# Optimization experiments

Measured on AMD Instinct MI355X. Metric: run time of the kernel, lower is better.

## Reference

```python
import jax, jax.numpy as jnp
import numpy as np

NUM_LEVELS = 4
SEARCH_RADIUS = 4
EPS = 1e-12  # torch F.normalize eps


def _avg_pool2d(x, s):
    # avg pool with kernel=stride=s over last two dims (exact, since H,W divisible by s)
    lead = x.shape[:-2]
    H, W = x.shape[-2], x.shape[-1]
    x = x.reshape(*lead, H // s, s, W // s, s)
    return x.mean(axis=(-3, -1))


def _l2_normalize(x, axis):
    n = jnp.sqrt(jnp.sum(x * x, axis=axis, keepdims=True))
    return x / jnp.maximum(n, EPS)


def _compute_correlation(query, values, radius):
    # query: [B,C,H,W], values: [B,N,C,H,W] -> [B,N,H,W,(2r+1)^2]
    q = _l2_normalize(query, axis=1)
    v = _l2_normalize(values, axis=2)
    corrs = []
    for dy in range(-radius, radius + 1):
        for dx in range(-radius, radius + 1):
            vs = v if (dy == 0 and dx == 0) else jnp.roll(v, (dy, dx), axis=(-2, -1))
            corrs.append(jnp.einsum('bchw,bnchw->bnhw', q, vs))
    return jnp.stack(corrs, axis=-1)


def setup_inputs() -> dict:
    key = jax.random.key(0)
    k1, k2, k3, k4 = jax.random.split(key, 4)
    B, N, C, H, W = 2, 4, 128, 160, 160
    Co = C // 2
    return {
        'query_feat': jax.random.normal(k1, (B, C, H, W), dtype=jnp.float32),
        'value_feats': jax.random.normal(k2, (B, N, C, H, W), dtype=jnp.float32),
        'proj_w': jax.random.normal(k3, (Co, C), dtype=jnp.float32) * (1.0 / np.sqrt(C)),
        'proj_b': jax.random.normal(k4, (Co,), dtype=jnp.float32) * 0.01,
    }


def reference(query_feat, value_feats, proj_w, proj_b):
    # 1x1 conv projection C -> C//2
    q = jnp.einsum('oc,bchw->bohw', proj_w, query_feat) + proj_b[None, :, None, None]
    v = jnp.einsum('oc,bnchw->bnohw', proj_w, value_feats) + proj_b[None, None, :, None, None]
    outs = []
    for level in range(NUM_LEVELS):
        scale = 2 ** level
        radius = max(1, SEARCH_RADIUS // scale)
        if scale > 1:
            q_l = _avg_pool2d(q, scale)
            v_l = _avg_pool2d(v, scale)
        else:
            q_l, v_l = q, v
        outs.append(_compute_correlation(q_l, v_l, radius))
    return tuple(outs)
```

## Files before the change

### kernel.cpp

```cpp
#include <hip/hip_runtime.h>


typedef _Float16 f16;
typedef _Float16 f16x4 __attribute__((ext_vector_type(4)));
typedef _Float16 f16x8 __attribute__((ext_vector_type(8)));
typedef float f32x4 __attribute__((ext_vector_type(4)));

#define EPSN 1e-12f

__global__ __launch_bounds__(256) void prep_weights(
    const float* __restrict__ wt, f16* __restrict__ wh) {
  int gid = blockIdx.x * 256 + threadIdx.x;
  float4 w = *(const float4*)(wt + gid * 4);
  f16x4 h;
  h[0] = (f16)w.x; h[1] = (f16)w.y; h[2] = (f16)w.z; h[3] = (f16)w.w;
  *(f16x4*)(wh + gid * 4) = h;
}

#define LROW 68
#define WS 136

__global__ __launch_bounds__(256, 3) void proj_pool(
    const float* __restrict__ xq, const float* __restrict__ xv,
    const f16* __restrict__ wh, const float* __restrict__ bias,
    f16* __restrict__ h0, f16* __restrict__ h1,
    f16* __restrict__ h2, f16* __restrict__ h3, int P) {
  __shared__ float xs[128 * LROW];
  __shared__ f16 wsh[64 * WS];
  float* accbuf = (float*)wsh;
  float* l3buf = xs;

  int bid = blockIdx.x;
  int img = bid / 400;
  int t = bid - img * 400;
  int ty = t / 20, tx = t - ty * 20;
  int py0 = ty * 8, px0 = tx * 8;
  const float* xsrc = (img < 2) ? (xq + (size_t)img * 128 * P)
                                : (xv + (size_t)(img - 2) * 128 * P);

  int tid = threadIdx.x;
  int lane = tid & 63;
  int wv = tid >> 6;
  int cl = lane & 15;
  int quad = lane >> 4;

  for (int m = tid; m < 1024; m += 256) {
    int o = m >> 4, kk = (m & 15) * 8;
    *(f16x8*)(wsh + o * WS + kk) = *(const f16x8*)(wh + o * 128 + kk);
  }

  {
    int cb = tid >> 4;
    int sub = tid & 15;
    int row = sub >> 1, hf = sub & 1;
#pragma unroll
    for (int i = 0; i < 8; ++i) {
      int c = cb + 16 * i;
      float4 v = *(const float4*)(xsrc + (size_t)c * P + (py0 + row) * 160 + px0 + hf * 4);
      int p = row * 8 + hf * 4;
      int x = (p + 8 * ((c >> 3) & 3)) & 63;
      *(float4*)(xs + c * LROW + x) = v;
    }
  }
  __syncthreads();

  f32x4 acc[4];
#pragma unroll
  for (int m = 0; m < 4; ++m) acc[m] = (f32x4)0.f;

  int pxl = wv * 16 + cl;
  int xr = (pxl + 8 * quad) & 63;

#pragma unroll
  for (int kc = 0; kc < 4; ++kc) {
    f16x8 bfr;
#pragma unroll
    for (int k = 0; k < 8; ++k) {
      int c = kc * 32 + quad * 8 + k;
      bfr[k] = (f16)xs[c * LROW + xr];
    }
    f16x8 afr[4];
#pragma unroll
    for (int mt = 0; mt < 4; ++mt)
      afr[mt] = *(const f16x8*)(wsh + (mt * 16 + cl) * WS + kc * 32 + quad * 8);
#pragma unroll
    for (int mt = 0; mt < 4; ++mt)
      acc[mt] = __builtin_amdgcn_mfma_f32_16x16x32_f16(afr[mt], bfr, acc[mt], 0, 0, 0);
  }

  float4 bi[4];
#pragma unroll
  for (int mt = 0; mt < 4; ++mt) bi[mt] = *(const float4*)(bias + mt * 16 + quad * 4);

  __syncthreads();

  float ss = 0.f;
#pragma unroll
  for (int mt = 0; mt < 4; ++mt) {
    acc[mt][0] += bi[mt].x;
    acc[mt][1] += bi[mt].y;
    acc[mt][2] += bi[mt].z;
    acc[mt][3] += bi[mt].w;
    *(float4*)(accbuf + pxl * LROW + mt * 16 + quad * 4) =
        make_float4(acc[mt][0], acc[mt][1], acc[mt][2], acc[mt][3]);
#pragma unroll
    for (int r = 0; r < 4; ++r) ss = fmaf(acc[mt][r], acc[mt][r], ss);
  }
  ss += __shfl_xor(ss, 16, 64);
  ss += __shfl_xor(ss, 32, 64);
  float s = 1.0f / fmaxf(sqrtf(ss), EPSN);
  {
    int gp = (py0 + (pxl >> 3)) * 160 + px0 + (pxl & 7);
    size_t base = ((size_t)img * P + gp) * 64;
#pragma unroll
    for (int mt = 0; mt < 4; ++mt) {
      f16x4 hn;
      hn[0] = (f16)(acc[mt][0] * s);
      hn[1] = (f16)(acc[mt][1] * s);
      hn[2] = (f16)(acc[mt][2] * s);
      hn[3] = (f16)(acc[mt][3] * s);
      *(f16x4*)(h0 + base + mt * 16 + quad * 4) = hn;
    }
  }
  __syncthreads();

  int r2 = wv >> 1, c2 = wv & 1;
  int g = quad, c4 = cl;
  int r1 = 2 * r2 + (g >> 1), c1 = 2 * c2 + (g & 1);
  int p00 = (2 * r1) * 8 + 2 * c1;

  float4 s00 = *(const float4*)(accbuf + p00 * LROW + c4 * 4);
  float4 s01 = *(const float4*)(accbuf + (p00 + 1) * LROW + c4 * 4);
  float4 s10 = *(const float4*)(accbuf + (p00 + 8) * LROW + c4 * 4);
  float4 s11 = *(const float4*)(accbuf + (p00 + 9) * LROW + c4 * 4);
  float4 v1;
  v1.x = 0.25f * (s00.x + s01.x + s10.x + s11.x);
  v1.y = 0.25f * (s00.y + s01.y + s10.y + s11.y);
  v1.z = 0.25f * (s00.z + s01.z + s10.z + s11.z);
  v1.w = 0.25f * (s00.w + s01.w + s10.w + s11.w);

  {
    float s1 = fmaf(v1.x, v1.x, fmaf(v1.y, v1.y, fmaf(v1.z, v1.z, v1.w * v1.w)));
    s1 += __shfl_xor(s1, 1, 64);
    s1 += __shfl_xor(s1, 2, 64);
    s1 += __shfl_xor(s1, 4, 64);
    s1 += __shfl_xor(s1, 8, 64);
    float sc = 1.0f / fmaxf(sqrtf(s1), EPSN);
    f16x4 h;
    h[0] = (f16)(v1.x * sc); h[1] = (f16)(v1.y * sc);
    h[2] = (f16)(v1.z * sc); h[3] = (f16)(v1.w * sc);
    *(f16x4*)(h1 + ((size_t)(img * 80 + ty * 4 + r1) * 80 + tx * 4 + c1) * 64 + c4 * 4) = h;
  }

  float4 q2v;
  q2v.x = v1.x + __shfl_xor(v1.x, 16, 64);
  q2v.y = v1.y + __shfl_xor(v1.y, 16, 64);
  q2v.z = v1.z + __shfl_xor(v1.z, 16, 64);
  q2v.w = v1.w + __shfl_xor(v1.w, 16, 64);
  q2v.x += __shfl_xor(q2v.x, 32, 64);
  q2v.y += __shfl_xor(q2v.y, 32, 64);
  q2v.z += __shfl_xor(q2v.z, 32, 64);
  q2v.w += __shfl_xor(q2v.w, 32, 64);
  q2v.x *= 0.25f; q2v.y *= 0.25f; q2v.z *= 0.25f; q2v.w *= 0.25f;

  {
    float s2 = fmaf(q2v.x, q2v.x, fmaf(q2v.y, q2v.y, fmaf(q2v.z, q2v.z, q2v.w * q2v.w)));
    s2 += __shfl_xor(s2, 1, 64);
    s2 += __shfl_xor(s2, 2, 64);
    s2 += __shfl_xor(s2, 4, 64);
    s2 += __shfl_xor(s2, 8, 64);
    float sc = 1.0f / fmaxf(sqrtf(s2), EPSN);
    if (g == 0) {
      f16x4 h;
      h[0] = (f16)(q2v.x * sc); h[1] = (f16)(q2v.y * sc);
      h[2] = (f16)(q2v.z * sc); h[3] = (f16)(q2v.w * sc);
      *(f16x4*)(h2 + ((size_t)(img * 40 + ty * 2 + r2) * 40 + tx * 2 + c2) * 64 + c4 * 4) = h;
      *(float4*)(l3buf + (wv * 16 + c4) * 4) = q2v;
    }
  }
  __syncthreads();

  if (tid < 16) {
    float4 a0 = *(const float4*)(l3buf + (0 * 16 + tid) * 4);
    float4 a1 = *(const float4*)(l3buf + (1 * 16 + tid) * 4);
    float4 a2 = *(const float4*)(l3buf + (2 * 16 + tid) * 4);
    float4 a3 = *(const float4*)(l3buf + (3 * 16 + tid) * 4);
    float4 q3;
    q3.x = 0.25f * (a0.x + a1.x + a2.x + a3.x);
    q3.y = 0.25f * (a0.y + a1.y + a2.y + a3.y);
    q3.z = 0.25f * (a0.z + a1.z + a2.z + a3.z);
    q3.w = 0.25f * (a0.w + a1.w + a2.w + a3.w);
    float s3 = fmaf(q3.x, q3.x, fmaf(q3.y, q3.y, fmaf(q3.z, q3.z, q3.w * q3.w)));
    s3 += __shfl_xor(s3, 1, 64);
    s3 += __shfl_xor(s3, 2, 64);
    s3 += __shfl_xor(s3, 4, 64);
    s3 += __shfl_xor(s3, 8, 64);
    float sc = 1.0f / fmaxf(sqrtf(s3), EPSN);
    f16x4 h;
    h[0] = (f16)(q3.x * sc); h[1] = (f16)(q3.y * sc);
    h[2] = (f16)(q3.z * sc); h[3] = (f16)(q3.w * sc);
    *(f16x4*)(h3 + ((size_t)(img * 20 + ty) * 20 + tx) * 64 + tid * 4) = h;
  }
}

template <int R>
__global__ __launch_bounds__(256, 4) void corr_mfma(
    const f16* __restrict__ qh, const f16* __restrict__ vh,
    float* __restrict__ out, int H, int W, int T) {
  constexpr int D = 2 * R + 1, DD = D * D;
  constexpr int PS = (DD + 3) & ~3;
  __shared__ float lw[4 * 16 * PS];

  int bn = blockIdx.x & 7;
  int wv = threadIdx.x >> 6;
  int widx = (blockIdx.x >> 3) * 4 + wv;
  int h = widx / T;
  int wt = widx - h * T;
  int lane = threadIdx.x & 63;
  int cl = lane & 15, quad = lane >> 4;
  int b = bn >> 2;
  int w0 = wt * 16;
  float* lwv = lw + wv * 16 * PS;

  int ap = w0 + cl; if (ap >= W) ap = W - 1;
  const f16* qp = qh + ((size_t)(b * H + h) * W + ap) * 64 + quad * 8;
  f16x8 a0 = *(const f16x8*)qp;
  f16x8 a1 = *(const f16x8*)(qp + 32);

  int c0 = w0 - R + cl; if (c0 < 0) c0 += W; if (c0 >= W) c0 -= W;
  int c1 = w0 + R + cl; if (c1 >= W) c1 -= W;
  int b0off = c0 * 64 + quad * 8;
  int b1off = c1 * 64 + quad * 8;

  int rbase = quad * 4;
  int base_dxi = rbase - cl + ((quad < 2) ? 2 * R : 0);

  for (int dyi = 0; dyi < D; ++dyi) {
    int h2 = h - dyi + R; if (h2 < 0) h2 += H; else if (h2 >= H) h2 -= H;
    const f16* vrow = vh + ((size_t)(bn * H + h2) * W) * 64;
    f16x8 b0a = *(const f16x8*)(vrow + b0off);
    f16x8 b0b = *(const f16x8*)(vrow + b0off + 32);
    f16x8 b1a = *(const f16x8*)(vrow + b1off);
    f16x8 b1b = *(const f16x8*)(vrow + b1off + 32);
    f32x4 A0 = __builtin_amdgcn_mfma_f32_16x16x32_f16(a0, b0a, (f32x4)0.f, 0, 0, 0);
    A0 = __builtin_amdgcn_mfma_f32_16x16x32_f16(a1, b0b, A0, 0, 0, 0);
    f32x4 A1 = __builtin_amdgcn_mfma_f32_16x16x32_f16(a0, b1a, (f32x4)0.f, 0, 0, 0);
    A1 = __builtin_amdgcn_mfma_f32_16x16x32_f16(a1, b1b, A1, 0, 0, 0);
#pragma unroll
    for (int rr = 0; rr < 4; ++rr) {
      int dxi = base_dxi + rr;
      float val = (quad < 2) ? A0[rr] : A1[rr];
      if ((unsigned)dxi <= (unsigned)(2 * R))
        lwv[(rbase + rr) * PS + dyi * D + dxi] = val;
    }
  }

  int vp = W - w0; if (vp > 16) vp = 16;
  float* ob = out + ((size_t)(bn * H + h) * W + w0) * DD;
  int tot = vp * DD;
  for (int gg = lane; gg < tot; gg += 64) {
    int pl = gg / DD;
    int rem = gg - pl * DD;
    ob[gg] = lwv[pl * PS + rem];
  }
}

extern "C" void kernel_launch(void* const* d_in, const int* in_sizes, int n_in,
                              void* d_out, int out_size, void* d_ws, size_t ws_size,
                              hipStream_t stream) {
  const float* query  = (const float*)d_in[0];
  const float* values = (const float*)d_in[1];
  const float* pw     = (const float*)d_in[2];
  const float* pb     = (const float*)d_in[3];
  float* out = (float*)d_out;
  float* ws  = (float*)d_ws;

  const int B = 2, N = 4;
  const int P0 = 160 * 160;

  f16* h0 = (f16*)ws;
  f16* h1 = h0 + (size_t)10 * P0 * 64;
  f16* h2 = h1 + (size_t)10 * (P0 / 4) * 64;
  f16* h3 = h2 + (size_t)10 * (P0 / 16) * 64;
  f16* wh = h3 + (size_t)10 * (P0 / 64) * 64;

  f16* q0h = h0;             f16* v0h = h0 + (size_t)2 * P0 * 64;
  f16* qh1 = h1;             f16* vh1 = h1 + (size_t)2 * (P0 / 4) * 64;
  f16* qh2 = h2;             f16* vh2 = h2 + (size_t)2 * (P0 / 16) * 64;
  f16* qh3 = h3;             f16* vh3 = h3 + (size_t)2 * (P0 / 64) * 64;

  prep_weights<<<8, 256, 0, stream>>>(pw, wh);

  proj_pool<<<4000, 256, 0, stream>>>(query, values, wh, pb, h0, h1, h2, h3, P0);

  float* out0 = out;
  float* out1 = out0 + (size_t)B * N * P0 * 81;
  float* out2 = out1 + (size_t)B * N * (P0 / 4) * 25;
  float* out3 = out2 + (size_t)B * N * (P0 / 16) * 9;
  corr_mfma<4><<<8 * 160 * 10 / 4, 256, 0, stream>>>(q0h, v0h, out0, 160, 160, 10);
  corr_mfma<2><<<8 * 80 * 5 / 4, 256, 0, stream>>>(qh1, vh1, out1, 80, 80, 5);
  corr_mfma<1><<<8 * 40 * 3 / 4, 256, 0, stream>>>(qh2, vh2, out2, 40, 40, 3);
  corr_mfma<1><<<8 * 20 * 2 / 4, 256, 0, stream>>>(qh3, vh3, out3, 20, 20, 2);
}
```

Before: 307.9 us.

## Fuse four correlation-level launches into one kernel and swizzle projection block order

Replaces the four per-level correlation launches with a single kernel that picks the pyramid level from the block index range, sharing one shared-memory buffer sized for the largest radius. This removes the launch gaps and tail idling between the small per-level grids and lets the small levels overlap with the large one. The projection kernel also remaps its block index so that consecutive hardware blocks are spread across images, which may change cache or channel locality. Occupancy hint raised to 6 blocks per CU, which may constrain registers.

```diff
diff --git a/kernel.cpp b/kernel.cpp
--- a/kernel.cpp
+++ b/kernel.cpp
@@ -30,7 +30,9 @@
   float* accbuf = (float*)wsh;
   float* l3buf = xs;
 
-  int bid = blockIdx.x;
+  int pb = blockIdx.x;
+  int bid = (pb & 7) * 500 + (pb >> 3);
+
   int img = bid / 400;
   int t = bid - img * 400;
   int ty = t / 20, tx = t - ty * 20;
@@ -204,16 +206,14 @@
 }
 
 template <int R>
-__global__ __launch_bounds__(256, 4) void corr_mfma(
+__device__ __forceinline__ void corr_level(
     const f16* __restrict__ qh, const f16* __restrict__ vh,
-    float* __restrict__ out, int H, int W, int T) {
+    float* __restrict__ out, int H, int W, int T, int blk, float* lw) {
   constexpr int D = 2 * R + 1, DD = D * D;
   constexpr int PS = (DD + 3) & ~3;
-  __shared__ float lw[4 * 16 * PS];
-
-  int bn = blockIdx.x & 7;
+  int bn = blk & 7;
   int wv = threadIdx.x >> 6;
-  int widx = (blockIdx.x >> 3) * 4 + wv;
+  int widx = (blk >> 3) * 4 + wv;
   int h = widx / T;
   int wt = widx - h * T;
   int lane = threadIdx.x & 63;
@@ -265,6 +265,21 @@
   }
 }
 
+__global__ __launch_bounds__(256, 6) void corr_all(
+    const f16* __restrict__ q0, const f16* __restrict__ v0,
+    const f16* __restrict__ q1, const f16* __restrict__ v1,
+    const f16* __restrict__ q2, const f16* __restrict__ v2,
+    const f16* __restrict__ q3, const f16* __restrict__ v3,
+    float* __restrict__ o0, float* __restrict__ o1,
+    float* __restrict__ o2, float* __restrict__ o3) {
+  __shared__ float lw[4 * 16 * 84];
+  int blk = blockIdx.x;
+  if (blk < 3200)      corr_level<4>(q0, v0, o0, 160, 160, 10, blk, lw);
+  else if (blk < 4000) corr_level<2>(q1, v1, o1, 80, 80, 5, blk - 3200, lw);
+  else if (blk < 4240) corr_level<1>(q2, v2, o2, 40, 40, 3, blk - 4000, lw);
+  else                 corr_level<1>(q3, v3, o3, 20, 20, 2, blk - 4240, lw);
+}
+
 extern "C" void kernel_launch(void* const* d_in, const int* in_sizes, int n_in,
                               void* d_out, int out_size, void* d_ws, size_t ws_size,
                               hipStream_t stream) {
@@ -297,8 +312,6 @@
   float* out1 = out0 + (size_t)B * N * P0 * 81;
   float* out2 = out1 + (size_t)B * N * (P0 / 4) * 25;
   float* out3 = out2 + (size_t)B * N * (P0 / 16) * 9;
-  corr_mfma<4><<<8 * 160 * 10 / 4, 256, 0, stream>>>(q0h, v0h, out0, 160, 160, 10);
-  corr_mfma<2><<<8 * 80 * 5 / 4, 256, 0, stream>>>(qh1, vh1, out1, 80, 80, 5);
-  corr_mfma<1><<<8 * 40 * 3 / 4, 256, 0, stream>>>(qh2, vh2, out2, 40, 40, 3);
-  corr_mfma<1><<<8 * 20 * 2 / 4, 256, 0, stream>>>(qh3, vh3, out3, 20, 20, 2);
-}
+  corr_all<<<4320, 256, 0, stream>>>(q0h, v0h, qh1, vh1, qh2, vh2, qh3, vh3,
+                                     out0, out1, out2, out3);
+}
```

Result: faster. 287.4 us (-6.7%).
